# Optimization experiments

Measured on AMD Instinct MI355X. Metric: run time of the kernel, lower is better.

Reference implementation:

```python
import jax, jax.numpy as jnp
import numpy as np

N_EMBD = 1024
N_HEADS = 16
HEAD_SIZE = N_EMBD // N_HEADS
B, T = 2, 2048


def setup_inputs() -> dict:
    key = jax.random.key(0)
    ks = jax.random.split(key, 6)
    s_in = 1.0 / np.sqrt(N_EMBD)
    x = jax.random.normal(ks[0], (B, T, N_EMBD), dtype=jnp.float32)
    # per-head projection weights, stored (H, C, Dh) = x @ W per head
    wq = jax.random.uniform(ks[1], (N_HEADS, N_EMBD, HEAD_SIZE), dtype=jnp.float32, minval=-s_in, maxval=s_in)
    wk = jax.random.uniform(ks[2], (N_HEADS, N_EMBD, HEAD_SIZE), dtype=jnp.float32, minval=-s_in, maxval=s_in)
    wv = jax.random.uniform(ks[3], (N_HEADS, N_EMBD, HEAD_SIZE), dtype=jnp.float32, minval=-s_in, maxval=s_in)
    # output projection (in, out) layout plus bias
    w_proj = jax.random.uniform(ks[4], (N_EMBD, N_EMBD), dtype=jnp.float32, minval=-s_in, maxval=s_in)
    b_proj = jax.random.uniform(ks[5], (N_EMBD,), dtype=jnp.float32, minval=-s_in, maxval=s_in)
    return {"x": x, "wq": wq, "wk": wk, "wv": wv, "w_proj": w_proj, "b_proj": b_proj}


def reference(x, wq, wk, wv, w_proj, b_proj):
    Bb, Tt, C = x.shape
    # all-head QKV projections in one einsum each: (B,T,C)x(H,C,Dh)->(B,H,T,Dh)
    q = jnp.einsum('btc,hcd->bhtd', x, wq)
    k = jnp.einsum('btc,hcd->bhtd', x, wk)
    v = jnp.einsum('btc,hcd->bhtd', x, wv)
    # NOTE: original scales by C**-0.5 with C = full n_embd, not head_size
    scores = jnp.einsum('bhtd,bhsd->bhts', q, k) * (C ** -0.5)
    causal = jnp.tril(jnp.ones((Tt, Tt), dtype=bool))  # is_decoder=True
    scores = jnp.where(causal, scores, -jnp.inf)
    wei = jax.nn.softmax(scores, axis=-1)
    out = jnp.einsum('bhts,bhsd->bhtd', wei, v)
    # concat heads: (B,H,T,Dh) -> (B,T,H*Dh)
    out = out.transpose(0, 2, 1, 3).reshape(Bb, Tt, C)
    return out @ w_proj + b_proj
```

## Files before the change

kernel.cpp:

```cpp
#include <hip/hip_runtime.h>


typedef unsigned short u16;
typedef unsigned int u32;

using bf16x8 = __attribute__((ext_vector_type(8))) short;
using bf16x4 = __attribute__((ext_vector_type(4))) short;
using f32x4  = __attribute__((ext_vector_type(4))) float;

#define T_SEQ 2048
#define C_DIM 1024
#define H_NUM 16
#define D_HEAD 64
#define NCHUNK 40

static __device__ inline f32x4 mfma16(bf16x8 a, bf16x8 b, f32x4 c) {
  return __builtin_amdgcn_mfma_f32_16x16x32_bf16(a, b, c, 0, 0, 0);
}

static __device__ inline short f2bf(float f) {
  union { float f; u32 u; } v; v.f = f;
  u32 u = v.u;
  return (short)((u + 0x7FFFu + ((u >> 16) & 1u)) >> 16);
}

static __device__ inline float bf2f(short s) {
  union { u32 u; float f; } v; v.u = ((u32)(u16)s) << 16;
  return v.f;
}

static __device__ inline float exp2_hw(float x) {
  return __builtin_amdgcn_exp2f(x);
}

static __device__ inline u32 cvtpk_bf16(float a, float b) {
  u32 r;
  asm("v_cvt_pk_bf16_f32 %0, %1, %2" : "=v"(r) : "v"(a), "v"(b));
  return r;
}

static __device__ inline void gload_lds16(const short* g, short* l) {
  __builtin_amdgcn_global_load_lds(
      (const __attribute__((address_space(1))) unsigned int*)g,
      (__attribute__((address_space(3))) unsigned int*)l,
      16, 0, 0);
}

__global__ __launch_bounds__(256) void ingest_kernel(
    const float* __restrict__ x, const float* __restrict__ wq,
    const float* __restrict__ wk, const float* __restrict__ wv,
    const float* __restrict__ wproj,
    short* __restrict__ xb, short* __restrict__ wt, short* __restrict__ wpT) {
  const int bid = blockIdx.x, t = threadIdx.x;
  if (bid < 4096) {
    size_t i4 = ((size_t)bid * 256 + t) * 4;
    const float4 v = *(const float4*)(x + i4);
    bf16x4 o4;
    o4[0] = f2bf(v.x); o4[1] = f2bf(v.y); o4[2] = f2bf(v.z); o4[3] = f2bf(v.w);
    *(bf16x4*)(xb + i4) = o4;
    return;
  }
  __shared__ short lt[64][72];
  const int rl = t >> 2, q16 = (t & 3) * 16;
  if (bid < 4864) {
    const int wb = bid - 4096;
    const int h3 = wb >> 4, c0 = (wb & 15) * 64;
    const float* w = (h3 < 16) ? wq : (h3 < 32) ? wk : wv;
    const int h = h3 & 15;
    const float* rp = w + (size_t)h * 65536 + (size_t)(c0 + rl) * 64 + q16;
#pragma unroll
    for (int j = 0; j < 16; j++) lt[rl][q16 + j] = f2bf(rp[j]);
    __syncthreads();
    short* op = wt + (size_t)h3 * 65536 + (size_t)rl * 1024 + c0 + q16;
#pragma unroll
    for (int j = 0; j < 16; j++) op[j] = lt[q16 + j][rl];
  } else {
    const int wc = bid - 4864;
    const int k0 = (wc >> 4) * 64, n0 = (wc & 15) * 64;
    const float* rp = wproj + (size_t)(k0 + rl) * 1024 + n0 + q16;
#pragma unroll
    for (int j = 0; j < 16; j++) lt[rl][q16 + j] = f2bf(rp[j]);
    __syncthreads();
    short* op = wpT + (size_t)(n0 + rl) * 1024 + k0 + q16;
#pragma unroll
    for (int j = 0; j < 16; j++) op[j] = lt[q16 + j][rl];
  }
}

__global__ __launch_bounds__(256) void qkv_kernel(
    const short* __restrict__ x, const short* __restrict__ wt,
    short* __restrict__ qo, short* __restrict__ ko, short* __restrict__ vto) {
  const int m0 = blockIdx.x * 128;
  const int n0 = blockIdx.y * 128;
  const int tid = threadIdx.x, w = tid >> 6, lane = tid & 63;
  const int l15 = lane & 15, quad = lane >> 4;
  const int wm = w >> 1, wn = w & 1;

  __shared__ __align__(16) short As[2][128 * 32];
  __shared__ __align__(16) short Bs[2][128 * 32];

  const int srow = w * 32 + (lane >> 2);
  const int skof = (lane & 3) * 8;
  const short* ga0 = x  + (size_t)(m0 + srow) * 1024 + skof;
  const short* ga1 = ga0 + 16 * 1024;
  const short* gb0 = wt + (size_t)(n0 + srow) * 1024 + skof;
  const short* gb1 = gb0 + 16 * 1024;
  const int lof0 = (w * 32) * 32;
  const int lof1 = (w * 32 + 16) * 32;

  f32x4 acc[4][4];
#pragma unroll
  for (int i = 0; i < 4; i++)
#pragma unroll
    for (int j = 0; j < 4; j++) acc[i][j] = f32x4{0, 0, 0, 0};

  const bool isv = (n0 >= 2048);

  auto stage = [&](int bi, int kt) {
    const int k0 = kt * 32;
    gload_lds16(ga0 + k0, &As[bi][lof0]);
    gload_lds16(ga1 + k0, &As[bi][lof1]);
    gload_lds16(gb0 + k0, &Bs[bi][lof0]);
    gload_lds16(gb1 + k0, &Bs[bi][lof1]);
  };
  auto compute = [&](int bi) {
    const short* ard = &As[bi][(wm * 64 + l15) * 32 + quad * 8];
    const short* brd = &Bs[bi][(wn * 64 + l15) * 32 + quad * 8];
    bf16x8 af[4], bfr[4];
#pragma unroll
    for (int i = 0; i < 4; i++) {
      af[i]  = *(const bf16x8*)(ard + i * 16 * 32);
      bfr[i] = *(const bf16x8*)(brd + i * 16 * 32);
    }
    if (!isv) {
#pragma unroll
      for (int mi = 0; mi < 4; mi++)
#pragma unroll
        for (int ni = 0; ni < 4; ni++)
          acc[mi][ni] = mfma16(af[mi], bfr[ni], acc[mi][ni]);
    } else {
#pragma unroll
      for (int ni = 0; ni < 4; ni++)
#pragma unroll
        for (int mi = 0; mi < 4; mi++)
          acc[ni][mi] = mfma16(bfr[ni], af[mi], acc[ni][mi]);
    }
  };

  stage(0, 0);
  __syncthreads();
#pragma unroll 1
  for (int kt2 = 0; kt2 < 16; kt2++) {
    stage(1, 2 * kt2 + 1);
    compute(0);
    __syncthreads();
    if (kt2 < 15) stage(0, 2 * kt2 + 2);
    compute(1);
    __syncthreads();
  }

  const int chunk = (n0 >> 6) + wn;
  const int sel = chunk >> 4, h = chunk & 15;
  if (!isv) {
    short* outp = (sel == 0) ? qo : ko;
    const float sc = (sel == 0) ? 0.045084441f : 1.0f;
#pragma unroll
    for (int mi = 0; mi < 4; mi++) {
#pragma unroll
      for (int r = 0; r < 4; r++) {
        int tg = m0 + wm * 64 + mi * 16 + quad * 4 + r;
        int b = tg >> 11, tl = tg & 2047;
        size_t rowb = ((size_t)(b * H_NUM + h) * T_SEQ + tl) * D_HEAD;
#pragma unroll
        for (int ni = 0; ni < 4; ni++)
          outp[rowb + ni * 16 + l15] = f2bf(acc[mi][ni][r] * sc);
      }
    }
  } else {
#pragma unroll
    for (int ni = 0; ni < 4; ni++) {
#pragma unroll
      for (int r = 0; r < 4; r++) {
        int d = ni * 16 + quad * 4 + r;
#pragma unroll
        for (int mi = 0; mi < 4; mi++) {
          int tg = m0 + wm * 64 + mi * 16 + l15;
          int b = tg >> 11, tl = tg & 2047;
          vto[((size_t)(b * H_NUM + h) * D_HEAD + d) * T_SEQ + tl] =
              f2bf(acc[ni][mi][r]);
        }
      }
    }
  }
}

__global__ __launch_bounds__(256) void attn_part_kernel(
    const short* __restrict__ q, const short* __restrict__ k,
    const short* __restrict__ vt, short* __restrict__ po,
    float* __restrict__ pl) {
  static const unsigned char order[NCHUNK] = {
      3, 4, 6, 8, 10, 11, 12, 13, 15, 16, 18, 19, 21, 22, 23, 24, 25, 26,
      28, 29, 30, 32, 33, 34, 36, 37, 38, 39,
      2, 9, 20, 35,
      1, 7, 17, 31,
      0, 5, 14, 27};
  static const unsigned char qtb_of[NCHUNK] = {
      0, 1, 2, 3, 4, 4, 5, 5, 6, 6, 7, 7, 8, 8, 8, 9, 9, 9, 10, 10,
      10, 11, 11, 11, 12, 12, 12, 12, 13, 13, 13, 13, 14, 14, 14, 14,
      15, 15, 15, 15};
  static const unsigned char base16[16] = {0, 1, 2, 3, 4, 6, 8, 10,
                                           12, 15, 18, 21, 24, 28, 32, 36};
  const int id = blockIdx.x;
  const int hb = id & 31;
  const int p  = id >> 5;
  const int pblk = order[p];
  const int qtb = qtb_of[pblk];
  const int sbeg = (pblk - base16[qtb]) * 512;
  const int send = min(sbeg + 512, (qtb + 1) * 128);

  const size_t bh = (size_t)hb;
  const short* qp = q  + bh * T_SEQ * D_HEAD;
  const short* kp = k  + bh * T_SEQ * D_HEAD;
  const short* vp = vt + bh * D_HEAD * T_SEQ;

  const int tid = threadIdx.x;
  const int w4 = tid >> 6;
  const int lane = tid & 63;
  const int l15 = lane & 15, quad = lane >> 4;
  const int swz8 = (l15 & 7) * 8;

  __shared__ __align__(16) short Ks[4096];
  __shared__ __align__(16) short Vs[4096];
  __shared__ __align__(16) short Ps[4][2048];
  short* pp = Ps[w4];

  const int q0w = qtb * 128 + w4 * 32;
  const int s_hi = min(send, ((qtb * 128 + 96 + 95) >> 6) << 6);

  const int srow = w4 * 16 + (lane >> 3);
  const int scol = ((lane & 7) ^ (lane >> 3)) * 8;
  const short* gK0 = kp + (size_t)(sbeg + srow) * 64 + scol;
  const short* gK1 = kp + (size_t)(sbeg + srow + 8) * 64 + scol;
  const short* gV0 = vp + (size_t)srow * 2048 + sbeg + scol;
  const short* gV1 = vp + (size_t)(srow + 8) * 2048 + sbeg + scol;
  short* lK0 = Ks + w4 * 1024 + lane * 8;
  short* lK1 = Ks + w4 * 1024 + 512 + lane * 8;
  short* lV0 = Vs + w4 * 1024 + lane * 8;
  short* lV1 = Vs + w4 * 1024 + 512 + lane * 8;

  auto stageKV = [&](int toff) {
    gload_lds16(gK0 + (size_t)toff * 64, lK0);
    gload_lds16(gK1 + (size_t)toff * 64, lK1);
    gload_lds16(gV0 + toff, lV0);
    gload_lds16(gV1 + toff, lV1);
  };

  const int rbase = l15 * 64;
  const int koff0 = (quad * 8) ^ swz8;
  const int koff1 = (32 + quad * 8) ^ swz8;

  bf16x8 qa[2][2];
#pragma unroll
  for (int h2 = 0; h2 < 2; h2++)
#pragma unroll
    for (int c2 = 0; c2 < 2; c2++)
      qa[h2][c2] = *(const bf16x8*)(qp + (size_t)(q0w + h2 * 16 + l15) * D_HEAD
                                    + c2 * 32 + quad * 8);

  f32x4 o[2][4];
#pragma unroll
  for (int h2 = 0; h2 < 2; h2++)
#pragma unroll
    for (int c = 0; c < 4; c++) o[h2][c] = f32x4{0, 0, 0, 0};
  float l_i[2] = { 0.f, 0.f };

  stageKV(0);

#pragma unroll 1
  for (int s0 = sbeg; s0 < s_hi; s0 += 64) {
    __syncthreads();

    f32x4 s[2][4];
    __builtin_amdgcn_s_setprio(1);
#pragma unroll
    for (int c = 0; c < 4; c++) {
      bf16x8 k0 = *(const bf16x8*)(Ks + c * 1024 + rbase + koff0);
      bf16x8 k1 = *(const bf16x8*)(Ks + c * 1024 + rbase + koff1);
#pragma unroll
      for (int h2 = 0; h2 < 2; h2++) {
        f32x4 z = { 0, 0, 0, 0 };
        z = mfma16(k0, qa[h2][0], z);
        z = mfma16(k1, qa[h2][1], z);
        s[h2][c] = z;
      }
    }
    __builtin_amdgcn_s_setprio(0);

    const bool needMask = (s0 + 64 > q0w);
#pragma unroll
    for (int h2 = 0; h2 < 2; h2++) {
      const int qg = q0w + h2 * 16 + l15;
      if (needMask) {
#pragma unroll
        for (int c = 0; c < 4; c++)
#pragma unroll
          for (int r = 0; r < 4; r++)
            if (s0 + c * 16 + quad * 4 + r > qg) s[h2][c][r] = -1e30f;
      }
      float rs = 0.f;
#pragma unroll
      for (int c = 0; c < 4; c++) {
#pragma unroll
        for (int r = 0; r < 4; r++) {
          float p2 = exp2_hw(s[h2][c][r]);
          s[h2][c][r] = p2;
          rs += p2;
        }
      }
      l_i[h2] += rs;
#pragma unroll
      for (int c = 0; c < 4; c++) {
        uint2 pw;
        pw.x = cvtpk_bf16(s[h2][c][0], s[h2][c][1]);
        pw.y = cvtpk_bf16(s[h2][c][2], s[h2][c][3]);
        *(uint2*)(pp + (h2 * 16 + l15) * 64 + ((c * 16 + quad * 4) ^ swz8)) = pw;
      }
    }
    asm volatile("" ::: "memory");

    __builtin_amdgcn_s_setprio(1);
#pragma unroll
    for (int kb2 = 0; kb2 < 2; kb2++) {
      const int ko = kb2 ? koff1 : koff0;
      bf16x8 pb0 = *(const bf16x8*)(pp + rbase + ko);
      bf16x8 pb1 = *(const bf16x8*)(pp + 1024 + rbase + ko);
#pragma unroll
      for (int c = 0; c < 4; c++) {
        bf16x8 va = *(const bf16x8*)(Vs + c * 1024 + rbase + ko);
        o[0][c] = mfma16(va, pb0, o[0][c]);
        o[1][c] = mfma16(va, pb1, o[1][c]);
      }
    }
    __builtin_amdgcn_s_setprio(0);

    __syncthreads();
    if (s0 + 64 < s_hi) stageKV(s0 + 64 - sbeg);
  }

  const size_t prow = (bh * NCHUNK + pblk) * 128;
#pragma unroll
  for (int h2 = 0; h2 < 2; h2++) {
    float lsum = l_i[h2];
    lsum += __shfl_xor(lsum, 16);
    lsum += __shfl_xor(lsum, 32);
    float inv = (lsum > 0.f) ? 1.0f / lsum : 0.f;
    int qlocal = w4 * 32 + h2 * 16 + l15;
    size_t rowoff = (prow + qlocal) * 64;
#pragma unroll
    for (int c = 0; c < 4; c++) {
      uint2 ow;
      ow.x = cvtpk_bf16(o[h2][c][0] * inv, o[h2][c][1] * inv);
      ow.y = cvtpk_bf16(o[h2][c][2] * inv, o[h2][c][3] * inv);
      *(uint2*)(&po[rowoff + c * 16 + quad * 4]) = ow;
    }
    if (quad == 0) pl[prow + qlocal] = lsum;
  }
}

__global__ __launch_bounds__(256) void attn_merge_kernel(
    const short* __restrict__ po, const float* __restrict__ pl,
    short* __restrict__ attnb) {
  static const unsigned char base16[16] = {0, 1, 2, 3, 4, 6, 8, 10,
                                           12, 15, 18, 21, 24, 28, 32, 36};
  int id = blockIdx.x * 256 + threadIdx.x;
  int dg = id & 7;
  int h  = (id >> 3) & 15;
  int t  = (id >> 7) & 2047;
  int b  = id >> 18;
  int qtb = t >> 7, ql = t & 127;
  int nch = (qtb >> 2) + 1;
  size_t bh = (size_t)(b * H_NUM + h);
  size_t r0 = (bh * NCHUNK + base16[qtb]) * 128 + ql;
  bf16x8 res;
  if (nch == 1) {
    res = *(const bf16x8*)(po + r0 * 64 + dg * 8);
  } else {
    float acc[8] = {0, 0, 0, 0, 0, 0, 0, 0};
    float lsum = 0.f;
    for (int c = 0; c < nch; c++) {
      size_t r = r0 + (size_t)c * 128;
      float lc = pl[r];
      lsum += lc;
      bf16x8 p = *(const bf16x8*)(po + r * 64 + dg * 8);
#pragma unroll
      for (int j = 0; j < 8; j++) acc[j] += lc * bf2f(p[j]);
    }
    float inv = 1.0f / lsum;
#pragma unroll
    for (int j = 0; j < 8; j++) res[j] = f2bf(acc[j] * inv);
  }
  *(bf16x8*)(&attnb[((size_t)(b * T_SEQ + t)) * C_DIM + h * D_HEAD + dg * 8]) = res;
}

__global__ __launch_bounds__(256) void proj_kernel(
    const short* __restrict__ a_in, const short* __restrict__ wpT,
    const float* __restrict__ bias, float* __restrict__ out) {
  const int m0 = blockIdx.x * 64;
  const int n0 = blockIdx.y * 128;
  const int tid = threadIdx.x, w = tid >> 6, lane = tid & 63;
  const int l15 = lane & 15, quad = lane >> 4;

  __shared__ __align__(16) short As[2][64 * 32];
  __shared__ __align__(16) short Bs[2][128 * 32];

  const short* gaA = a_in + (size_t)(m0 + w * 16 + (lane >> 2)) * 1024
                     + (lane & 3) * 8;
  const int lofA = w * 16 * 32;
  const int srowB = w * 32 + (lane >> 2);
  const short* gb0 = wpT + (size_t)(n0 + srowB) * 1024 + (lane & 3) * 8;
  const short* gb1 = gb0 + 16 * 1024;
  const int lof0 = (w * 32) * 32;
  const int lof1 = (w * 32 + 16) * 32;

  f32x4 acc[4][2];
#pragma unroll
  for (int i = 0; i < 4; i++)
#pragma unroll
    for (int j = 0; j < 2; j++) acc[i][j] = f32x4{0, 0, 0, 0};

  auto stage = [&](int bi, int kt) {
    const int k0 = kt * 32;
    gload_lds16(gaA + k0, &As[bi][lofA]);
    gload_lds16(gb0 + k0, &Bs[bi][lof0]);
    gload_lds16(gb1 + k0, &Bs[bi][lof1]);
  };
  auto compute = [&](int bi) {
    const short* ard = &As[bi][l15 * 32 + quad * 8];
    const short* brd = &Bs[bi][(w * 32 + l15) * 32 + quad * 8];
    bf16x8 af[4], bfr[2];
#pragma unroll
    for (int i = 0; i < 4; i++)
      af[i] = *(const bf16x8*)(ard + i * 16 * 32);
#pragma unroll
    for (int j = 0; j < 2; j++)
      bfr[j] = *(const bf16x8*)(brd + j * 16 * 32);
#pragma unroll
    for (int mi = 0; mi < 4; mi++)
#pragma unroll
      for (int ni = 0; ni < 2; ni++)
        acc[mi][ni] = mfma16(af[mi], bfr[ni], acc[mi][ni]);
  };

  stage(0, 0);
  __syncthreads();
#pragma unroll 1
  for (int kt2 = 0; kt2 < 16; kt2++) {
    stage(1, 2 * kt2 + 1);
    compute(0);
    __syncthreads();
    if (kt2 < 15) stage(0, 2 * kt2 + 2);
    compute(1);
    __syncthreads();
  }

#pragma unroll
  for (int mi = 0; mi < 4; mi++) {
#pragma unroll
    for (int r = 0; r < 4; r++) {
      int mq = m0 + mi * 16 + quad * 4 + r;
#pragma unroll
      for (int ni = 0; ni < 2; ni++) {
        int n = n0 + w * 32 + ni * 16 + l15;
        out[(size_t)mq * C_DIM + n] = acc[mi][ni][r] + bias[n];
      }
    }
  }
}

extern "C" void kernel_launch(void* const* d_in, const int* in_sizes, int n_in,
                              void* d_out, int out_size, void* d_ws, size_t ws_size,
                              hipStream_t stream) {
  const float* x     = (const float*)d_in[0];
  const float* wq    = (const float*)d_in[1];
  const float* wk    = (const float*)d_in[2];
  const float* wv    = (const float*)d_in[3];
  const float* wproj = (const float*)d_in[4];
  const float* bias  = (const float*)d_in[5];

  short* ws = (short*)d_ws;
  short* wpT    = ws;
  short* qb     = ws + 1048576;
  short* wt_qkv = ws + 9437184;
  short* xb     = ws + 12582912;
  short* po     = ws + 5242880;
  float* pl     = (float*)(ws + 15728640);
  short* attnb  = ws + 1048576;
  short* kb     = (short*)d_out;
  short* vtb    = (short*)d_out + 4194304;

  ingest_kernel<<<5120, 256, 0, stream>>>(x, wq, wk, wv, wproj, xb, wt_qkv, wpT);
  qkv_kernel<<<dim3(32, 24), 256, 0, stream>>>(xb, wt_qkv, qb, kb, vtb);
  attn_part_kernel<<<NCHUNK * 32, 256, 0, stream>>>(qb, kb, vtb, po, pl);
  attn_merge_kernel<<<2048, 256, 0, stream>>>(po, pl, attnb);
  proj_kernel<<<dim3(64, 8), 256, 0, stream>>>(attnb, wpT, bias, (float*)d_out);
}
```

Before: 190.9 us.

## Restructure QKV GEMM into 256x256 tiles with triple-buffered interleaved pipeline

Result: slower. 253.5 us (+32.8%).

```diff
diff --git a/kernel.cpp b/kernel.cpp
--- a/kernel.cpp
+++ b/kernel.cpp
@@ -87,77 +87,136 @@
   }
 }
 
-__global__ __launch_bounds__(256) void qkv_kernel(
+__global__ __launch_bounds__(512) void qkv_kernel(
     const short* __restrict__ x, const short* __restrict__ wt,
     short* __restrict__ qo, short* __restrict__ ko, short* __restrict__ vto) {
-  const int m0 = blockIdx.x * 128;
-  const int n0 = blockIdx.y * 128;
-  const int tid = threadIdx.x, w = tid >> 6, lane = tid & 63;
+  const int bid = blockIdx.x;
+  const int m0 = (bid & 15) * 256;
+  const int n0 = (bid >> 4) * 256;
+  const int t = threadIdx.x;
+  const int wid = t >> 6, lane = t & 63;
+  const int wm = wid >> 2, wn = wid & 3;
   const int l15 = lane & 15, quad = lane >> 4;
-  const int wm = w >> 1, wn = w & 1;
-
-  __shared__ __align__(16) short As[2][128 * 32];
-  __shared__ __align__(16) short Bs[2][128 * 32];
-
-  const int srow = w * 32 + (lane >> 2);
-  const int skof = (lane & 3) * 8;
-  const short* ga0 = x  + (size_t)(m0 + srow) * 1024 + skof;
-  const short* ga1 = ga0 + 16 * 1024;
-  const short* gb0 = wt + (size_t)(n0 + srow) * 1024 + skof;
-  const short* gb1 = gb0 + 16 * 1024;
-  const int lof0 = (w * 32) * 32;
-  const int lof1 = (w * 32 + 16) * 32;
-
-  f32x4 acc[4][4];
-#pragma unroll
-  for (int i = 0; i < 4; i++)
+  const bool isv = (n0 >= 2048);
+
+  __shared__ __align__(16) short Abuf[3][8192];
+  __shared__ __align__(16) short Bbuf[3][8192];
+
+  const short* baseA = x  + (size_t)(m0 + (t >> 2)) * 1024 + (t & 3) * 8;
+  const short* baseB = wt + (size_t)(n0 + (t >> 2)) * 1024 + (t & 3) * 8;
+  const int dstT = t * 8;
+
+  f32x4 acc[8][4];
+#pragma unroll
+  for (int i = 0; i < 8; i++)
 #pragma unroll
     for (int j = 0; j < 4; j++) acc[i][j] = f32x4{0, 0, 0, 0};
 
-  const bool isv = (n0 >= 2048);
-
-  auto stage = [&](int bi, int kt) {
-    const int k0 = kt * 32;
-    gload_lds16(ga0 + k0, &As[bi][lof0]);
-    gload_lds16(ga1 + k0, &As[bi][lof1]);
-    gload_lds16(gb0 + k0, &Bs[bi][lof0]);
-    gload_lds16(gb1 + k0, &Bs[bi][lof1]);
-  };
-  auto compute = [&](int bi) {
-    const short* ard = &As[bi][(wm * 64 + l15) * 32 + quad * 8];
-    const short* brd = &Bs[bi][(wn * 64 + l15) * 32 + quad * 8];
-    bf16x8 af[4], bfr[4];
-#pragma unroll
-    for (int i = 0; i < 4; i++) {
-      af[i]  = *(const bf16x8*)(ard + i * 16 * 32);
-      bfr[i] = *(const bf16x8*)(brd + i * 16 * 32);
-    }
-    if (!isv) {
-#pragma unroll
-      for (int mi = 0; mi < 4; mi++)
-#pragma unroll
-        for (int ni = 0; ni < 4; ni++)
-          acc[mi][ni] = mfma16(af[mi], bfr[ni], acc[mi][ni]);
-    } else {
-#pragma unroll
-      for (int ni = 0; ni < 4; ni++)
-#pragma unroll
-        for (int mi = 0; mi < 4; mi++)
-          acc[ni][mi] = mfma16(bfr[ni], af[mi], acc[ni][mi]);
-    }
-  };
-
-  stage(0, 0);
-  __syncthreads();
+  bf16x8 bf_[4];
+
+  const int aoff = (wm * 128 + l15) * 32 + quad * 8;
+  const int boff = (wn * 64 + l15) * 32 + quad * 8;
+
+#define QKV_P0(cur, kt2, doIssue)                                           \
+  {                                                                         \
+    bf16x8 af[4];                                                           \
+    _Pragma("unroll")                                                       \
+    for (int i = 0; i < 4; i++)                                             \
+      af[i] = *(const bf16x8*)(Abuf[cur] + aoff + i * 512);                 \
+    _Pragma("unroll")                                                       \
+    for (int j = 0; j < 4; j++)                                             \
+      bf_[j] = *(const bf16x8*)(Bbuf[cur] + boff + j * 512);                \
+    if (doIssue) {                                                          \
+      gload_lds16(baseA + (kt2) * 32, Abuf[(kt2) % 3] + dstT);              \
+      gload_lds16(baseA + 131072 + (kt2) * 32,                              \
+                  Abuf[(kt2) % 3] + 4096 + dstT);                           \
+    }                                                                       \
+    asm volatile("s_waitcnt lgkmcnt(0)" ::: "memory");                      \
+    __builtin_amdgcn_sched_barrier(0);                                      \
+    __builtin_amdgcn_s_setprio(1);                                          \
+    if (!isv) {                                                             \
+      _Pragma("unroll")                                                     \
+      for (int mi = 0; mi < 4; mi++)                                        \
+        _Pragma("unroll")                                                   \
+        for (int ni = 0; ni < 4; ni++)                                      \
+          acc[mi][ni] = mfma16(af[mi], bf_[ni], acc[mi][ni]);               \
+    } else {                                                                \
+      _Pragma("unroll")                                                     \
+      for (int ni = 0; ni < 4; ni++)                                        \
+        _Pragma("unroll")                                                   \
+        for (int mi = 0; mi < 4; mi++)                                      \
+          acc[mi][ni] = mfma16(bf_[ni], af[mi], acc[mi][ni]);               \
+    }                                                                       \
+    __builtin_amdgcn_s_setprio(0);                                          \
+  }
+
+#define QKV_P1(cur, kt2, doIssue)                                           \
+  {                                                                         \
+    bf16x8 af[4];                                                           \
+    _Pragma("unroll")                                                       \
+    for (int i = 0; i < 4; i++)                                             \
+      af[i] = *(const bf16x8*)(Abuf[cur] + aoff + (i + 4) * 512);           \
+    if (doIssue) {                                                          \
+      gload_lds16(baseB + (kt2) * 32, Bbuf[(kt2) % 3] + dstT);              \
+      gload_lds16(baseB + 131072 + (kt2) * 32,                              \
+                  Bbuf[(kt2) % 3] + 4096 + dstT);                           \
+    }                                                                       \
+    asm volatile("s_waitcnt lgkmcnt(0)" ::: "memory");                      \
+    __builtin_amdgcn_sched_barrier(0);                                      \
+    __builtin_amdgcn_s_setprio(1);                                          \
+    if (!isv) {                                                             \
+      _Pragma("unroll")                                                     \
+      for (int mi = 0; mi < 4; mi++)                                        \
+        _Pragma("unroll")                                                   \
+        for (int ni = 0; ni < 4; ni++)                                      \
+          acc[mi + 4][ni] = mfma16(af[mi], bf_[ni], acc[mi + 4][ni]);       \
+    } else {                                                                \
+      _Pragma("unroll")                                                     \
+      for (int ni = 0; ni < 4; ni++)                                        \
+        _Pragma("unroll")                                                   \
+        for (int mi = 0; mi < 4; mi++)                                      \
+          acc[mi + 4][ni] = mfma16(bf_[ni], af[mi], acc[mi + 4][ni]);       \
+    }                                                                       \
+    __builtin_amdgcn_s_setprio(0);                                          \
+  }
+
+  gload_lds16(baseA, Abuf[0] + dstT);
+  gload_lds16(baseA + 131072, Abuf[0] + 4096 + dstT);
+  gload_lds16(baseB, Bbuf[0] + dstT);
+  gload_lds16(baseB + 131072, Bbuf[0] + 4096 + dstT);
+  gload_lds16(baseA + 32, Abuf[1] + dstT);
+  gload_lds16(baseA + 131072 + 32, Abuf[1] + 4096 + dstT);
+  gload_lds16(baseB + 32, Bbuf[1] + dstT);
+  gload_lds16(baseB + 131072 + 32, Bbuf[1] + 4096 + dstT);
+  asm volatile("s_waitcnt vmcnt(4)" ::: "memory");
+  __builtin_amdgcn_s_barrier();
+  asm volatile("" ::: "memory");
+
 #pragma unroll 1
-  for (int kt2 = 0; kt2 < 16; kt2++) {
-    stage(1, 2 * kt2 + 1);
-    compute(0);
-    __syncthreads();
-    if (kt2 < 15) stage(0, 2 * kt2 + 2);
-    compute(1);
-    __syncthreads();
-  }
+  for (int kt = 0; kt < 30; kt++) {
+    const int cur = kt % 3;
+    QKV_P0(cur, kt + 2, true)
+    __builtin_amdgcn_s_barrier();
+    asm volatile("" ::: "memory");
+    QKV_P1(cur, kt + 2, true)
+    asm volatile("s_waitcnt vmcnt(4)" ::: "memory");
+    __builtin_amdgcn_s_barrier();
+    asm volatile("" ::: "memory");
+  }
+  QKV_P0(0, 0, false)
+  __builtin_amdgcn_s_barrier();
+  asm volatile("" ::: "memory");
+  QKV_P1(0, 0, false)
+  asm volatile("s_waitcnt vmcnt(0)" ::: "memory");
+  __builtin_amdgcn_s_barrier();
+  asm volatile("" ::: "memory");
+  QKV_P0(1, 0, false)
+  __builtin_amdgcn_s_barrier();
+  asm volatile("" ::: "memory");
+  QKV_P1(1, 0, false)
+
+#undef QKV_P0
+#undef QKV_P1
 
   const int chunk = (n0 >> 6) + wn;
   const int sel = chunk >> 4, h = chunk & 15;
@@ -165,10 +224,10 @@
     short* outp = (sel == 0) ? qo : ko;
     const float sc = (sel == 0) ? 0.045084441f : 1.0f;
 #pragma unroll
-    for (int mi = 0; mi < 4; mi++) {
+    for (int mi = 0; mi < 8; mi++) {
 #pragma unroll
       for (int r = 0; r < 4; r++) {
-        int tg = m0 + wm * 64 + mi * 16 + quad * 4 + r;
+        int tg = m0 + wm * 128 + mi * 16 + quad * 4 + r;
         int b = tg >> 11, tl = tg & 2047;
         size_t rowb = ((size_t)(b * H_NUM + h) * T_SEQ + tl) * D_HEAD;
 #pragma unroll
@@ -183,11 +242,11 @@
       for (int r = 0; r < 4; r++) {
         int d = ni * 16 + quad * 4 + r;
 #pragma unroll
-        for (int mi = 0; mi < 4; mi++) {
-          int tg = m0 + wm * 64 + mi * 16 + l15;
+        for (int mi = 0; mi < 8; mi++) {
+          int tg = m0 + wm * 128 + mi * 16 + l15;
           int b = tg >> 11, tl = tg & 2047;
           vto[((size_t)(b * H_NUM + h) * D_HEAD + d) * T_SEQ + tl] =
-              f2bf(acc[ni][mi][r]);
+              f2bf(acc[mi][ni][r]);
         }
       }
     }
@@ -499,7 +558,7 @@
   short* vtb    = (short*)d_out + 4194304;
 
   ingest_kernel<<<5120, 256, 0, stream>>>(x, wq, wk, wv, wproj, xb, wt_qkv, wpT);
-  qkv_kernel<<<dim3(32, 24), 256, 0, stream>>>(xb, wt_qkv, qb, kb, vtb);
+  qkv_kernel<<<192, 512, 0, stream>>>(xb, wt_qkv, qb, kb, vtb);
   attn_part_kernel<<<NCHUNK * 32, 256, 0, stream>>>(qb, kb, vtb, po, pl);
   attn_merge_kernel<<<2048, 256, 0, stream>>>(po, pl, attnb);
   proj_kernel<<<dim3(64, 8), 256, 0, stream>>>(attnb, wpT, bias, (float*)d_out);
```
